# Kernel tuning notes

Measured on AMD Instinct MI355X. Metric: run time of the kernel, lower is better.

The kernel has to match this reference:

```python
import jax, jax.numpy as jnp
import numpy as np


def _gru_layer(x, h0, W_ih, W_hh, b_ih, b_hh):
    # x: [B, T, D_in], h0: [B, H]; PyTorch gate order (r, z, n)
    xg = jnp.einsum('btd,gd->btg', x, W_ih) + b_ih  # [B, T, 3H] input projections, hoisted out of scan

    def step(h, xg_t):
        gh = h @ W_hh.T + b_hh                      # [B, 3H]
        xr, xz, xn = jnp.split(xg_t, 3, axis=-1)
        hr, hz, hn = jnp.split(gh, 3, axis=-1)
        r = jax.nn.sigmoid(xr + hr)
        z = jax.nn.sigmoid(xz + hz)
        n = jnp.tanh(xn + r * hn)
        h_new = (1.0 - z) * n + z * h
        return h_new, h_new

    hT, ys = jax.lax.scan(step, h0, jnp.swapaxes(xg, 0, 1))  # scan over time
    return jnp.swapaxes(ys, 0, 1), hT  # outputs [B, T, H], final hidden [B, H]


def setup_inputs() -> dict:
    key = jax.random.key(0)
    ks = jax.random.split(key, 14)
    B, T, D, H, C = 256, 256, 128, 512, 10
    s_in = 1.0 / np.sqrt(H)  # PyTorch GRU init scale (uniform bound); use scaled normals
    inp = {
        'x': jax.random.normal(ks[0], (B, T, D), jnp.float32),
        'W_ih0': jax.random.normal(ks[1], (3 * H, D), jnp.float32) * s_in,
        'W_hh0': jax.random.normal(ks[2], (3 * H, H), jnp.float32) * s_in,
        'b_ih0': jax.random.normal(ks[3], (3 * H,), jnp.float32) * s_in,
        'b_hh0': jax.random.normal(ks[4], (3 * H,), jnp.float32) * s_in,
        'W_ih1': jax.random.normal(ks[5], (3 * H, H), jnp.float32) * s_in,
        'W_hh1': jax.random.normal(ks[6], (3 * H, H), jnp.float32) * s_in,
        'b_ih1': jax.random.normal(ks[7], (3 * H,), jnp.float32) * s_in,
        'b_hh1': jax.random.normal(ks[8], (3 * H,), jnp.float32) * s_in,
        'fc1_w': jax.random.normal(ks[9], (128, H), jnp.float32) * s_in,
        'fc1_b': jax.random.normal(ks[10], (128,), jnp.float32) * s_in,
        'fc2_w': jax.random.normal(ks[11], (C, 128), jnp.float32) * (1.0 / np.sqrt(128)),
        'fc2_b': jax.random.normal(ks[12], (C,), jnp.float32) * (1.0 / np.sqrt(128)),
    }
    return inp


def reference(x, W_ih0, W_hh0, b_ih0, b_hh0, W_ih1, W_hh1, b_ih1, b_hh1, fc1_w, fc1_b, fc2_w, fc2_b):
    B = x.shape[0]
    H = W_hh0.shape[1]
    h0 = jnp.zeros((B, H), x.dtype)
    # layer 0
    y0, _ = _gru_layer(x, h0, W_ih0, W_hh0, b_ih0, b_hh0)
    # layer 1 (dropout inactive at inference)
    _, hT1 = _gru_layer(y0, h0, W_ih1, W_hh1, b_ih1, b_hh1)
    out = jax.nn.relu(hT1)                # relu on last layer's final hidden state
    out = jax.nn.relu(out @ fc1_w.T + fc1_b)
    out = out @ fc2_w.T + fc2_b           # [B, num_classes]
    return out
```

## Files before the change

kernel.cpp:

```cpp
#include <hip/hip_runtime.h>
#include <hip/hip_fp16.h>


#define B_  256
#define T_  256
#define D_  128
#define H_  512
#define G3  1536
#define BH  (B_ * H_)

typedef _Float16 h8  __attribute__((ext_vector_type(8)));
typedef _Float16 h2v __attribute__((ext_vector_type(2)));
typedef float    f4  __attribute__((ext_vector_type(4)));

#define MFMA16(a, b, c) __builtin_amdgcn_mfma_f32_16x16x32_f16((a), (b), (c), 0, 0, 0)

__device__ __forceinline__ int swz(int c, int r) { return (c & ~7) | ((c + r) & 7); }

__device__ __forceinline__ float sigmoid_f(float v) { return 1.f / (1.f + __expf(-v)); }
__device__ __forceinline__ float tanh_f(float v) {
    float ex = __expf(2.f * v);
    return 1.f - 2.f / (ex + 1.f);
}

__device__ __forceinline__ void ld8_sc(
    const _Float16* p0, const _Float16* p1, const _Float16* p2, const _Float16* p3,
    const _Float16* p4, const _Float16* p5, const _Float16* p6, const _Float16* p7,
    h8& r0, h8& r1, h8& r2, h8& r3, h8& r4, h8& r5, h8& r6, h8& r7) {
    asm volatile(
        "global_load_dwordx4 %0, %8, off sc0 sc1\n\t"
        "global_load_dwordx4 %1, %9, off sc0 sc1\n\t"
        "global_load_dwordx4 %2, %10, off sc0 sc1\n\t"
        "global_load_dwordx4 %3, %11, off sc0 sc1\n\t"
        "global_load_dwordx4 %4, %12, off sc0 sc1\n\t"
        "global_load_dwordx4 %5, %13, off sc0 sc1\n\t"
        "global_load_dwordx4 %6, %14, off sc0 sc1\n\t"
        "global_load_dwordx4 %7, %15, off sc0 sc1\n\t"
        "s_waitcnt vmcnt(0)"
        : "=&v"(r0), "=&v"(r1), "=&v"(r2), "=&v"(r3),
          "=&v"(r4), "=&v"(r5), "=&v"(r6), "=&v"(r7)
        : "v"(p0), "v"(p1), "v"(p2), "v"(p3),
          "v"(p4), "v"(p5), "v"(p6), "v"(p7)
        : "memory");
}
__device__ __forceinline__ void ld4_sc(
    const _Float16* p0, const _Float16* p1, const _Float16* p2, const _Float16* p3,
    h8& r0, h8& r1, h8& r2, h8& r3) {
    asm volatile(
        "global_load_dwordx4 %0, %4, off sc0 sc1\n\t"
        "global_load_dwordx4 %1, %5, off sc0 sc1\n\t"
        "global_load_dwordx4 %2, %6, off sc0 sc1\n\t"
        "global_load_dwordx4 %3, %7, off sc0 sc1\n\t"
        "s_waitcnt vmcnt(0)"
        : "=&v"(r0), "=&v"(r1), "=&v"(r2), "=&v"(r3)
        : "v"(p0), "v"(p1), "v"(p2), "v"(p3)
        : "memory");
}
__device__ __forceinline__ void st16_sc(_Float16* p, h8 v) {
    asm volatile("global_store_dwordx4 %0, %1, off sc0 sc1" :: "v"(p), "v"(v) : "memory");
}

__global__ void convert_weights(const float* __restrict__ Wih0,
                                const float* __restrict__ Whh0,
                                const float* __restrict__ Wih1,
                                const float* __restrict__ Whh1,
                                _Float16* __restrict__ Wcat0,
                                _Float16* __restrict__ Wcat1) {
    int g = blockIdx.x;
    for (int k = threadIdx.x; k < D_; k += blockDim.x)
        Wcat0[(size_t)g * 640 + k] = (_Float16)Wih0[(size_t)g * D_ + k];
    for (int k = threadIdx.x; k < H_; k += blockDim.x) {
        Wcat0[(size_t)g * 640 + 128 + k]  = (_Float16)Whh0[(size_t)g * H_ + k];
        Wcat1[(size_t)g * 1024 + k]       = (_Float16)Wih1[(size_t)g * H_ + k];
        Wcat1[(size_t)g * 1024 + 512 + k] = (_Float16)Whh1[(size_t)g * H_ + k];
    }
}

__global__ __launch_bounds__(256, 1) void gru_fused(
    const float* __restrict__ x,
    const _Float16* __restrict__ Wcat0, const _Float16* __restrict__ Wcat1,
    const float* __restrict__ bih0, const float* __restrict__ bhh0,
    const float* __restrict__ bih1, const float* __restrict__ bhh1,
    _Float16* __restrict__ h0ring,
    _Float16* __restrict__ h1ring,
    float* __restrict__ hT,
    int* __restrict__ flagbase) {
    __shared__ __attribute__((aligned(16))) _Float16 As[16 * 1152];
    __shared__ float ghp[4][16][100];
    __shared__ float anx[16][32];

    const int tid  = threadIdx.x;
    const int bg   = blockIdx.x & 15;
    const int cg   = blockIdx.x >> 4;
    const int wave = tid >> 6;
    const int lane = tid & 63;
    const int l15  = lane & 15;
    const int q    = lane >> 4;
    const int b0   = bg * 16;
    const int hc0  = cg * 32;
    int* flags = flagbase + bg * 16;

    h8 wf0[5][6];
#pragma unroll
    for (int s = 0; s < 5; ++s) {
        const int kh = (wave * 5 + s) * 32 + q * 8;
#pragma unroll
        for (int nt = 0; nt < 6; ++nt) {
            const int grow = (nt >> 1) * H_ + hc0 + (nt & 1) * 16 + l15;
            wf0[s][nt] = *(const h8*)(Wcat0 + (size_t)grow * 640 + kh);
        }
    }
    h8 wf1[8][6];
#pragma unroll
    for (int s = 0; s < 8; ++s) {
        const int kh = (wave * 8 + s) * 32 + q * 8;
#pragma unroll
        for (int nt = 0; nt < 6; ++nt) {
            const int grow = (nt >> 1) * H_ + hc0 + (nt & 1) * 16 + l15;
            wf1[s][nt] = *(const h8*)(Wcat1 + (size_t)grow * 1024 + kh);
        }
    }
    float br0[2], bz0[2], bi0[2], bh0[2], br1[2], bz1[2], bi1[2], bh1[2];
    {
        const int jj = (tid & 15) * 2;
#pragma unroll
        for (int e = 0; e < 2; ++e) {
            const int col = hc0 + jj + e;
            br0[e] = bih0[col] + bhh0[col];
            bz0[e] = bih0[H_ + col] + bhh0[H_ + col];
            bi0[e] = bih0[2 * H_ + col];
            bh0[e] = bhh0[2 * H_ + col];
            br1[e] = bih1[col] + bhh1[col];
            bz1[e] = bih1[H_ + col] + bhh1[H_ + col];
            bi1[e] = bih1[2 * H_ + col];
            bh1[e] = bhh1[2 * H_ + col];
        }
    }

#pragma unroll 1
    for (int u = 0; u <= T_; ++u) {
        {
            const int r = tid >> 4, c16 = tid & 15;
            if (u < T_) {
                const float* xp = x + ((size_t)(b0 + r) * T_ + u) * D_ + c16 * 8;
                float4 v0 = *(const float4*)(xp);
                float4 v1 = *(const float4*)(xp + 4);
                h8 hx;
                hx[0] = (_Float16)v0.x; hx[1] = (_Float16)v0.y;
                hx[2] = (_Float16)v0.z; hx[3] = (_Float16)v0.w;
                hx[4] = (_Float16)v1.x; hx[5] = (_Float16)v1.y;
                hx[6] = (_Float16)v1.z; hx[7] = (_Float16)v1.w;
                *(h8*)&As[r * 1152 + swz(c16, r) * 8] = hx;
            }
            const _Float16* h0p = h0ring + (size_t)((u + 1) & 1) * BH + (size_t)(b0 + r) * H_;
            const _Float16* h1p = h1ring + (size_t)(u & 1) * BH + (size_t)(b0 + r) * H_;
            h8 a0 = {}, a1 = {}, a2 = {}, a3 = {}, c0 = {}, c1 = {}, c2 = {}, c3 = {};
            if (u > 1) {
                ld8_sc(h0p + c16 * 8, h0p + (c16 + 16) * 8, h0p + (c16 + 32) * 8, h0p + (c16 + 48) * 8,
                       h1p + c16 * 8, h1p + (c16 + 16) * 8, h1p + (c16 + 32) * 8, h1p + (c16 + 48) * 8,
                       a0, a1, a2, a3, c0, c1, c2, c3);
            } else if (u == 1) {
                ld4_sc(h0p + c16 * 8, h0p + (c16 + 16) * 8, h0p + (c16 + 32) * 8, h0p + (c16 + 48) * 8,
                       a0, a1, a2, a3);
            }
            *(h8*)&As[r * 1152 + swz(16 + c16,      r) * 8] = a0;
            *(h8*)&As[r * 1152 + swz(16 + c16 + 16, r) * 8] = a1;
            *(h8*)&As[r * 1152 + swz(16 + c16 + 32, r) * 8] = a2;
            *(h8*)&As[r * 1152 + swz(16 + c16 + 48, r) * 8] = a3;
            *(h8*)&As[r * 1152 + swz(80 + c16,      r) * 8] = c0;
            *(h8*)&As[r * 1152 + swz(80 + c16 + 16, r) * 8] = c1;
            *(h8*)&As[r * 1152 + swz(80 + c16 + 32, r) * 8] = c2;
            *(h8*)&As[r * 1152 + swz(80 + c16 + 48, r) * 8] = c3;
        }
        __syncthreads();
        if (u < T_) {
            f4 arz0 = {0,0,0,0}, arz1 = {0,0,0,0}, arz2 = {0,0,0,0}, arz3 = {0,0,0,0};
            f4 anx0 = {0,0,0,0}, anx1 = {0,0,0,0}, anh0 = {0,0,0,0}, anh1 = {0,0,0,0};
#pragma unroll
            for (int s = 0; s < 5; ++s) {
                const int kstep = wave * 5 + s;
                const int c = kstep * 4 + q;
                h8 a = *(const h8*)&As[l15 * 1152 + swz(c, l15) * 8];
                arz0 = MFMA16(a, wf0[s][0], arz0);
                arz1 = MFMA16(a, wf0[s][1], arz1);
                arz2 = MFMA16(a, wf0[s][2], arz2);
                arz3 = MFMA16(a, wf0[s][3], arz3);
                if (kstep < 4) {
                    anx0 = MFMA16(a, wf0[s][4], anx0);
                    anx1 = MFMA16(a, wf0[s][5], anx1);
                } else {
                    anh0 = MFMA16(a, wf0[s][4], anh0);
                    anh1 = MFMA16(a, wf0[s][5], anh1);
                }
            }
#pragma unroll
            for (int i = 0; i < 4; ++i) {
                float* row = &ghp[wave][q * 4 + i][0];
                row[ 0 + l15] = arz0[i];
                row[16 + l15] = arz1[i];
                row[32 + l15] = arz2[i];
                row[48 + l15] = arz3[i];
                row[64 + l15] = anh0[i];
                row[80 + l15] = anh1[i];
            }
            if (wave == 0) {
#pragma unroll
                for (int i = 0; i < 4; ++i) {
                    anx[q * 4 + i][l15]      = anx0[i];
                    anx[q * 4 + i][16 + l15] = anx1[i];
                }
            }
        }
        __syncthreads();
        if (u < T_) {
            const int er = tid >> 4;
            const int jj = (tid & 15) * 2;
            h2v out2;
#pragma unroll
            for (int e = 0; e < 2; ++e) {
                const int j = jj + e;
                float gr = 0.f, gz = 0.f, ghn = 0.f;
#pragma unroll
                for (int w = 0; w < 4; ++w) {
                    gr  += ghp[w][er][j];
                    gz  += ghp[w][er][32 + j];
                    ghn += ghp[w][er][64 + j];
                }
                const float gxn = anx[er][j];
                const float rr = sigmoid_f(gr + br0[e]);
                const float zz = sigmoid_f(gz + bz0[e]);
                const float nn = tanh_f(gxn + bi0[e] + rr * (ghn + bh0[e]));
                const int hcol = hc0 + j;
                const float hp = (float)As[er * 1152 + swz(16 + (hcol >> 3), er) * 8 + (hcol & 7)];
                out2[e] = (_Float16)((1.f - zz) * nn + zz * hp);
            }
            *(h2v*)&As[er * 1152 + swz(jj >> 3, er) * 8 + (jj & 7)] = out2;
        }
        __syncthreads();
        if (wave == 0 && u < T_) {
            const int row = lane >> 2, ch = lane & 3;
            h8 v = *(const h8*)&As[row * 1152 + swz(ch, row) * 8];
            st16_sc(h0ring + (size_t)(u & 1) * BH + (size_t)(b0 + row) * H_ + hc0 + ch * 8, v);
        }
        if (u > 0) {
            f4 arz0 = {0,0,0,0}, arz1 = {0,0,0,0}, arz2 = {0,0,0,0}, arz3 = {0,0,0,0};
            f4 an0 = {0,0,0,0}, an1 = {0,0,0,0};
#pragma unroll
            for (int s = 0; s < 8; ++s) {
                const int c = 16 + (wave * 8 + s) * 4 + q;
                h8 a = *(const h8*)&As[l15 * 1152 + swz(c, l15) * 8];
                arz0 = MFMA16(a, wf1[s][0], arz0);
                arz1 = MFMA16(a, wf1[s][1], arz1);
                arz2 = MFMA16(a, wf1[s][2], arz2);
                arz3 = MFMA16(a, wf1[s][3], arz3);
                an0  = MFMA16(a, wf1[s][4], an0);
                an1  = MFMA16(a, wf1[s][5], an1);
            }
#pragma unroll
            for (int i = 0; i < 4; ++i) {
                float* row = &ghp[wave][q * 4 + i][0];
                row[ 0 + l15] = arz0[i];
                row[16 + l15] = arz1[i];
                row[32 + l15] = arz2[i];
                row[48 + l15] = arz3[i];
                row[64 + l15] = an0[i];
                row[80 + l15] = an1[i];
            }
        }
        __syncthreads();
        if (u > 0) {
            const int er = tid >> 4;
            const int jj = (tid & 15) * 2;
            h2v out2;
            float hvf[2];
#pragma unroll
            for (int e = 0; e < 2; ++e) {
                const int j = jj + e;
                float gr = 0.f, gz = 0.f;
#pragma unroll
                for (int w = 0; w < 4; ++w) {
                    gr += ghp[w][er][j];
                    gz += ghp[w][er][32 + j];
                }
                const float gxn = ghp[0][er][64 + j] + ghp[1][er][64 + j];
                const float ghn = ghp[2][er][64 + j] + ghp[3][er][64 + j];
                const float rr = sigmoid_f(gr + br1[e]);
                const float zz = sigmoid_f(gz + bz1[e]);
                const float nn = tanh_f(gxn + bi1[e] + rr * (ghn + bh1[e]));
                const int hcol = hc0 + j;
                const float hp = (float)As[er * 1152 + swz(80 + (hcol >> 3), er) * 8 + (hcol & 7)];
                hvf[e] = (1.f - zz) * nn + zz * hp;
                out2[e] = (_Float16)hvf[e];
            }
            const int hcol0 = hc0 + jj;
            *(h2v*)&As[er * 1152 + swz(80 + (hcol0 >> 3), er) * 8 + (hcol0 & 7)] = out2;
            if (u == T_) {
                hT[(size_t)(b0 + er) * H_ + hc0 + jj]     = hvf[0];
                hT[(size_t)(b0 + er) * H_ + hc0 + jj + 1] = hvf[1];
            }
        }
        if (u < T_) {
            __syncthreads();
            if (wave == 0) {
                if (u > 0) {
                    const int row = lane >> 2, ch = lane & 3;
                    const int gch = 80 + (hc0 >> 3) + ch;
                    h8 v = *(const h8*)&As[row * 1152 + swz(gch, row) * 8];
                    st16_sc(h1ring + (size_t)((u + 1) & 1) * BH + (size_t)(b0 + row) * H_ + hc0 + ch * 8, v);
                }
                asm volatile("s_waitcnt vmcnt(0)" ::: "memory");
                if (lane == 0)
                    __hip_atomic_store(flags + cg, u + 1, __ATOMIC_RELAXED, __HIP_MEMORY_SCOPE_AGENT);
                int ok;
                do {
                    __builtin_amdgcn_s_sleep(1);
                    int f = 0x7fffffff;
                    if (lane < 16)
                        f = __hip_atomic_load(flags + lane, __ATOMIC_RELAXED, __HIP_MEMORY_SCOPE_AGENT);
                    ok = __all(f >= u + 1);
                } while (!ok);
            }
            __syncthreads();
        }
    }
}

__global__ __launch_bounds__(128) void head_kernel(
    const float* __restrict__ hT, const float* __restrict__ fc1_w,
    const float* __restrict__ fc1_b, const float* __restrict__ fc2_w,
    const float* __restrict__ fc2_b, float* __restrict__ out) {
    __shared__ float hs[512];
    __shared__ float a1[128];
    const int b = blockIdx.x, tid = threadIdx.x;
    for (int k = tid; k < H_; k += 128) {
        float v = hT[(size_t)b * H_ + k];
        hs[k] = v > 0.f ? v : 0.f;
    }
    __syncthreads();
    float acc = fc1_b[tid];
    const float* wr = fc1_w + (size_t)tid * H_;
    for (int k = 0; k < H_; k += 4) {
        float4 w = *(const float4*)(wr + k);
        acc += w.x * hs[k] + w.y * hs[k + 1] + w.z * hs[k + 2] + w.w * hs[k + 3];
    }
    a1[tid] = acc > 0.f ? acc : 0.f;
    __syncthreads();
    if (tid < 10) {
        float o = fc2_b[tid];
        const float* w2 = fc2_w + (size_t)tid * 128;
        for (int k = 0; k < 128; ++k) o += w2[k] * a1[k];
        out[(size_t)b * 10 + tid] = o;
    }
}

extern "C" void kernel_launch(void* const* d_in, const int* in_sizes, int n_in,
                              void* d_out, int out_size, void* d_ws, size_t ws_size,
                              hipStream_t stream) {
    const float* x    = (const float*)d_in[0];
    const float* Wih0 = (const float*)d_in[1];
    const float* Whh0 = (const float*)d_in[2];
    const float* bih0 = (const float*)d_in[3];
    const float* bhh0 = (const float*)d_in[4];
    const float* Wih1 = (const float*)d_in[5];
    const float* Whh1 = (const float*)d_in[6];
    const float* bih1 = (const float*)d_in[7];
    const float* bhh1 = (const float*)d_in[8];
    const float* fc1w = (const float*)d_in[9];
    const float* fc1b = (const float*)d_in[10];
    const float* fc2w = (const float*)d_in[11];
    const float* fc2b = (const float*)d_in[12];

    char* ws = (char*)d_ws;
    size_t off = 0;
    int* flags = (int*)(ws + off); off += 16 * 16 * 4;
    off = (off + 255) & ~(size_t)255;
    _Float16* Wcat0 = (_Float16*)(ws + off); off += (size_t)G3 * 640 * 2;
    off = (off + 255) & ~(size_t)255;
    _Float16* Wcat1 = (_Float16*)(ws + off); off += (size_t)G3 * 1024 * 2;
    off = (off + 255) & ~(size_t)255;
    _Float16* h0ring = (_Float16*)(ws + off); off += (size_t)2 * BH * 2;
    _Float16* h1ring = (_Float16*)(ws + off); off += (size_t)2 * BH * 2;
    float* hT = (float*)(ws + off); off += (size_t)BH * 4;

    hipMemsetAsync(flags, 0, 16 * 16 * 4, stream);

    hipLaunchKernelGGL(convert_weights, dim3(G3), dim3(256), 0, stream,
                       Wih0, Whh0, Wih1, Whh1, Wcat0, Wcat1);
    hipLaunchKernelGGL(gru_fused, dim3(256), dim3(256), 0, stream,
                       x, Wcat0, Wcat1, bih0, bhh0, bih1, bhh1,
                       h0ring, h1ring, hT, flags);
    hipLaunchKernelGGL(head_kernel, dim3(B_), dim3(128), 0, stream,
                       hT, fc1w, fc1b, fc2w, fc2b, (float*)d_out);
}
```

Before: 1.313 ms.

## Split per-layer sync flags and prefetch next-step hidden states before barrier

Replaces the single per-step flag barrier with separate layer-0 and layer-1 flags. Layer 0 publishes its flag right after storing h0, so dependent blocks can start loading h0 while layer 1 is still finishing. The next step's h0, h1 and x loads are issued at the end of the iteration and waited on at the top of the next, overlapping load latency with the second flag wait. This adds an extra spin-wait and a memset of h1ring, and relies on relaxed atomics for ordering the ring-buffer reads.

```diff
diff --git a/kernel.cpp b/kernel.cpp
--- a/kernel.cpp
+++ b/kernel.cpp
@@ -23,35 +23,14 @@
     return 1.f - 2.f / (ex + 1.f);
 }
 
-__device__ __forceinline__ void ld8_sc(
-    const _Float16* p0, const _Float16* p1, const _Float16* p2, const _Float16* p3,
-    const _Float16* p4, const _Float16* p5, const _Float16* p6, const _Float16* p7,
-    h8& r0, h8& r1, h8& r2, h8& r3, h8& r4, h8& r5, h8& r6, h8& r7) {
-    asm volatile(
-        "global_load_dwordx4 %0, %8, off sc0 sc1\n\t"
-        "global_load_dwordx4 %1, %9, off sc0 sc1\n\t"
-        "global_load_dwordx4 %2, %10, off sc0 sc1\n\t"
-        "global_load_dwordx4 %3, %11, off sc0 sc1\n\t"
-        "global_load_dwordx4 %4, %12, off sc0 sc1\n\t"
-        "global_load_dwordx4 %5, %13, off sc0 sc1\n\t"
-        "global_load_dwordx4 %6, %14, off sc0 sc1\n\t"
-        "global_load_dwordx4 %7, %15, off sc0 sc1\n\t"
-        "s_waitcnt vmcnt(0)"
-        : "=&v"(r0), "=&v"(r1), "=&v"(r2), "=&v"(r3),
-          "=&v"(r4), "=&v"(r5), "=&v"(r6), "=&v"(r7)
-        : "v"(p0), "v"(p1), "v"(p2), "v"(p3),
-          "v"(p4), "v"(p5), "v"(p6), "v"(p7)
-        : "memory");
-}
-__device__ __forceinline__ void ld4_sc(
+__device__ __forceinline__ void ld4_issue(
     const _Float16* p0, const _Float16* p1, const _Float16* p2, const _Float16* p3,
     h8& r0, h8& r1, h8& r2, h8& r3) {
     asm volatile(
         "global_load_dwordx4 %0, %4, off sc0 sc1\n\t"
         "global_load_dwordx4 %1, %5, off sc0 sc1\n\t"
         "global_load_dwordx4 %2, %6, off sc0 sc1\n\t"
-        "global_load_dwordx4 %3, %7, off sc0 sc1\n\t"
-        "s_waitcnt vmcnt(0)"
+        "global_load_dwordx4 %3, %7, off sc0 sc1"
         : "=&v"(r0), "=&v"(r1), "=&v"(r2), "=&v"(r3)
         : "v"(p0), "v"(p1), "v"(p2), "v"(p3)
         : "memory");
@@ -84,7 +63,8 @@
     _Float16* __restrict__ h0ring,
     _Float16* __restrict__ h1ring,
     float* __restrict__ hT,
-    int* __restrict__ flagbase) {
+    int* __restrict__ flag0base,
+    int* __restrict__ flag1base) {
     __shared__ __attribute__((aligned(16))) _Float16 As[16 * 1152];
     __shared__ float ghp[4][16][100];
     __shared__ float anx[16][32];
@@ -98,7 +78,8 @@
     const int q    = lane >> 4;
     const int b0   = bg * 16;
     const int hc0  = cg * 32;
-    int* flags = flagbase + bg * 16;
+    int* f0g = flag0base + bg * 16;
+    int* f1g = flag1base + bg * 16;
 
     h8 wf0[5][6];
 #pragma unroll
@@ -137,41 +118,38 @@
         }
     }
 
+    const int r   = tid >> 4;
+    const int c16 = tid & 15;
+
+    h8 p0 = {}, p1 = {}, p2 = {}, p3 = {};
+    h8 q0 = {}, q1 = {}, q2 = {}, q3 = {};
+    float4 vx0 = {0,0,0,0}, vx1 = {0,0,0,0};
+
+    {
+        const float* xp = x + ((size_t)(b0 + r) * T_ + 0) * D_ + c16 * 8;
+        vx0 = *(const float4*)(xp);
+        vx1 = *(const float4*)(xp + 4);
+    }
+
 #pragma unroll 1
     for (int u = 0; u <= T_; ++u) {
-        {
-            const int r = tid >> 4, c16 = tid & 15;
-            if (u < T_) {
-                const float* xp = x + ((size_t)(b0 + r) * T_ + u) * D_ + c16 * 8;
-                float4 v0 = *(const float4*)(xp);
-                float4 v1 = *(const float4*)(xp + 4);
-                h8 hx;
-                hx[0] = (_Float16)v0.x; hx[1] = (_Float16)v0.y;
-                hx[2] = (_Float16)v0.z; hx[3] = (_Float16)v0.w;
-                hx[4] = (_Float16)v1.x; hx[5] = (_Float16)v1.y;
-                hx[6] = (_Float16)v1.z; hx[7] = (_Float16)v1.w;
-                *(h8*)&As[r * 1152 + swz(c16, r) * 8] = hx;
-            }
-            const _Float16* h0p = h0ring + (size_t)((u + 1) & 1) * BH + (size_t)(b0 + r) * H_;
-            const _Float16* h1p = h1ring + (size_t)(u & 1) * BH + (size_t)(b0 + r) * H_;
-            h8 a0 = {}, a1 = {}, a2 = {}, a3 = {}, c0 = {}, c1 = {}, c2 = {}, c3 = {};
-            if (u > 1) {
-                ld8_sc(h0p + c16 * 8, h0p + (c16 + 16) * 8, h0p + (c16 + 32) * 8, h0p + (c16 + 48) * 8,
-                       h1p + c16 * 8, h1p + (c16 + 16) * 8, h1p + (c16 + 32) * 8, h1p + (c16 + 48) * 8,
-                       a0, a1, a2, a3, c0, c1, c2, c3);
-            } else if (u == 1) {
-                ld4_sc(h0p + c16 * 8, h0p + (c16 + 16) * 8, h0p + (c16 + 32) * 8, h0p + (c16 + 48) * 8,
-                       a0, a1, a2, a3);
-            }
-            *(h8*)&As[r * 1152 + swz(16 + c16,      r) * 8] = a0;
-            *(h8*)&As[r * 1152 + swz(16 + c16 + 16, r) * 8] = a1;
-            *(h8*)&As[r * 1152 + swz(16 + c16 + 32, r) * 8] = a2;
-            *(h8*)&As[r * 1152 + swz(16 + c16 + 48, r) * 8] = a3;
-            *(h8*)&As[r * 1152 + swz(80 + c16,      r) * 8] = c0;
-            *(h8*)&As[r * 1152 + swz(80 + c16 + 16, r) * 8] = c1;
-            *(h8*)&As[r * 1152 + swz(80 + c16 + 32, r) * 8] = c2;
-            *(h8*)&As[r * 1152 + swz(80 + c16 + 48, r) * 8] = c3;
-        }
+        asm volatile("s_waitcnt vmcnt(0)" ::: "memory");
+        if (u < T_) {
+            h8 hx;
+            hx[0] = (_Float16)vx0.x; hx[1] = (_Float16)vx0.y;
+            hx[2] = (_Float16)vx0.z; hx[3] = (_Float16)vx0.w;
+            hx[4] = (_Float16)vx1.x; hx[5] = (_Float16)vx1.y;
+            hx[6] = (_Float16)vx1.z; hx[7] = (_Float16)vx1.w;
+            *(h8*)&As[r * 1152 + swz(c16, r) * 8] = hx;
+        }
+        *(h8*)&As[r * 1152 + swz(16 + c16,      r) * 8] = p0;
+        *(h8*)&As[r * 1152 + swz(16 + c16 + 16, r) * 8] = p1;
+        *(h8*)&As[r * 1152 + swz(16 + c16 + 32, r) * 8] = p2;
+        *(h8*)&As[r * 1152 + swz(16 + c16 + 48, r) * 8] = p3;
+        *(h8*)&As[r * 1152 + swz(80 + c16,      r) * 8] = q0;
+        *(h8*)&As[r * 1152 + swz(80 + c16 + 16, r) * 8] = q1;
+        *(h8*)&As[r * 1152 + swz(80 + c16 + 32, r) * 8] = q2;
+        *(h8*)&As[r * 1152 + swz(80 + c16 + 48, r) * 8] = q3;
         __syncthreads();
         if (u < T_) {
             f4 arz0 = {0,0,0,0}, arz1 = {0,0,0,0}, arz2 = {0,0,0,0}, arz3 = {0,0,0,0};
@@ -213,8 +191,8 @@
         }
         __syncthreads();
         if (u < T_) {
-            const int er = tid >> 4;
-            const int jj = (tid & 15) * 2;
+            const int er = r;
+            const int jj = c16 * 2;
             h2v out2;
 #pragma unroll
             for (int e = 0; e < 2; ++e) {
@@ -241,6 +219,9 @@
             const int row = lane >> 2, ch = lane & 3;
             h8 v = *(const h8*)&As[row * 1152 + swz(ch, row) * 8];
             st16_sc(h0ring + (size_t)(u & 1) * BH + (size_t)(b0 + row) * H_ + hc0 + ch * 8, v);
+            asm volatile("s_waitcnt vmcnt(0)" ::: "memory");
+            if (lane == 0)
+                __hip_atomic_store(f0g + cg, u + 1, __ATOMIC_RELAXED, __HIP_MEMORY_SCOPE_AGENT);
         }
         if (u > 0) {
             f4 arz0 = {0,0,0,0}, arz1 = {0,0,0,0}, arz2 = {0,0,0,0}, arz3 = {0,0,0,0};
@@ -269,8 +250,8 @@
         }
         __syncthreads();
         if (u > 0) {
-            const int er = tid >> 4;
-            const int jj = (tid & 15) * 2;
+            const int er = r;
+            const int jj = c16 * 2;
             h2v out2;
             float hvf[2];
 #pragma unroll
@@ -299,28 +280,52 @@
                 hT[(size_t)(b0 + er) * H_ + hc0 + jj + 1] = hvf[1];
             }
         }
+        __syncthreads();
         if (u < T_) {
-            __syncthreads();
-            if (wave == 0) {
-                if (u > 0) {
-                    const int row = lane >> 2, ch = lane & 3;
-                    const int gch = 80 + (hc0 >> 3) + ch;
-                    h8 v = *(const h8*)&As[row * 1152 + swz(gch, row) * 8];
-                    st16_sc(h1ring + (size_t)((u + 1) & 1) * BH + (size_t)(b0 + row) * H_ + hc0 + ch * 8, v);
-                }
+            if (wave == 0 && u > 0) {
+                const int row = lane >> 2, ch = lane & 3;
+                const int gch = 80 + (hc0 >> 3) + ch;
+                h8 v = *(const h8*)&As[row * 1152 + swz(gch, row) * 8];
+                st16_sc(h1ring + (size_t)((u + 1) & 1) * BH + (size_t)(b0 + row) * H_ + hc0 + ch * 8, v);
                 asm volatile("s_waitcnt vmcnt(0)" ::: "memory");
                 if (lane == 0)
-                    __hip_atomic_store(flags + cg, u + 1, __ATOMIC_RELAXED, __HIP_MEMORY_SCOPE_AGENT);
-                int ok;
+                    __hip_atomic_store(f1g + cg, u, __ATOMIC_RELAXED, __HIP_MEMORY_SCOPE_AGENT);
+            }
+            {
+                int fv;
                 do {
+                    fv = (lane < 16) ? __hip_atomic_load(f0g + lane, __ATOMIC_RELAXED, __HIP_MEMORY_SCOPE_AGENT)
+                                     : 0x7fffffff;
+                    if (__all(fv >= u + 1)) break;
                     __builtin_amdgcn_s_sleep(1);
-                    int f = 0x7fffffff;
-                    if (lane < 16)
-                        f = __hip_atomic_load(flags + lane, __ATOMIC_RELAXED, __HIP_MEMORY_SCOPE_AGENT);
-                    ok = __all(f >= u + 1);
-                } while (!ok);
-            }
-            __syncthreads();
+                } while (true);
+            }
+            {
+                const _Float16* h0p = h0ring + (size_t)(u & 1) * BH + (size_t)(b0 + r) * H_;
+                ld4_issue(h0p + c16 * 8, h0p + (c16 + 16) * 8,
+                          h0p + (c16 + 32) * 8, h0p + (c16 + 48) * 8,
+                          p0, p1, p2, p3);
+            }
+            {
+                int fv;
+                do {
+                    fv = (lane < 16) ? __hip_atomic_load(f1g + lane, __ATOMIC_RELAXED, __HIP_MEMORY_SCOPE_AGENT)
+                                     : 0x7fffffff;
+                    if (__all(fv >= u)) break;
+                    __builtin_amdgcn_s_sleep(1);
+                } while (true);
+            }
+            {
+                const _Float16* h1p = h1ring + (size_t)((u + 1) & 1) * BH + (size_t)(b0 + r) * H_;
+                ld4_issue(h1p + c16 * 8, h1p + (c16 + 16) * 8,
+                          h1p + (c16 + 32) * 8, h1p + (c16 + 48) * 8,
+                          q0, q1, q2, q3);
+                if (u + 1 < T_) {
+                    const float* xp = x + ((size_t)(b0 + r) * T_ + (u + 1)) * D_ + c16 * 8;
+                    vx0 = *(const float4*)(xp);
+                    vx1 = *(const float4*)(xp + 4);
+                }
+            }
         }
     }
 }
@@ -372,7 +377,8 @@
 
     char* ws = (char*)d_ws;
     size_t off = 0;
-    int* flags = (int*)(ws + off); off += 16 * 16 * 4;
+    int* flags0 = (int*)(ws + off); off += 16 * 16 * 4;
+    int* flags1 = (int*)(ws + off); off += 16 * 16 * 4;
     off = (off + 255) & ~(size_t)255;
     _Float16* Wcat0 = (_Float16*)(ws + off); off += (size_t)G3 * 640 * 2;
     off = (off + 255) & ~(size_t)255;
@@ -382,13 +388,14 @@
     _Float16* h1ring = (_Float16*)(ws + off); off += (size_t)2 * BH * 2;
     float* hT = (float*)(ws + off); off += (size_t)BH * 4;
 
-    hipMemsetAsync(flags, 0, 16 * 16 * 4, stream);
+    (void)hipMemsetAsync(flags0, 0, 2 * 16 * 16 * 4, stream);
+    (void)hipMemsetAsync(h1ring, 0, (size_t)2 * BH * 2, stream);
 
     hipLaunchKernelGGL(convert_weights, dim3(G3), dim3(256), 0, stream,
                        Wih0, Whh0, Wih1, Whh1, Wcat0, Wcat1);
     hipLaunchKernelGGL(gru_fused, dim3(256), dim3(256), 0, stream,
                        x, Wcat0, Wcat1, bih0, bhh0, bih1, bhh1,
-                       h0ring, h1ring, hT, flags);
+                       h0ring, h1ring, hT, flags0, flags1);
     hipLaunchKernelGGL(head_kernel, dim3(B_), dim3(128), 0, stream,
                        hT, fc1w, fc1b, fc2w, fc2b, (float*)d_out);
 }
```

Result: slower. 1.672 ms (+27.3%).
